# Kernel tuning notes

Measured on AMD Instinct MI355X. Metric: run time of the kernel, lower is better.

## Reference

```python
import jax, jax.numpy as jnp
import numpy as np

N_CLASSES = 91  # classes 0..90; class 0 (background) is excluded from the mean


def setup_inputs() -> dict:
    key = jax.random.key(0)
    k1, k2 = jax.random.split(key)
    B, H, W = 64, 512, 512
    # label maps with integer class ids in [0, 91); `inputs` stored as float32
    # to mirror the original (compared elementwise against integer i)
    inputs = jax.random.randint(k1, (B, H, W), 0, N_CLASSES).astype(jnp.float32)
    targets = jax.random.randint(k2, (B, H, W), 0, N_CLASSES).astype(jnp.int32)
    return {"inputs": inputs, "targets": targets, "smooth": 1}


def reference(inputs, targets, smooth):
    # Single-pass histogram formulation of the original per-class loop:
    #   intersection_i = #{p : inputs[p]==i and targets[p]==i}
    #   total_i        = #{inputs==i} + #{targets==i}
    #   union_i        = total_i - intersection_i
    n = N_CLASSES
    inp = inputs.reshape(-1).astype(jnp.int32)
    tgt = targets.reshape(-1).astype(jnp.int32)
    cnt_in = jnp.bincount(inp, length=n).astype(jnp.float32)
    cnt_tg = jnp.bincount(tgt, length=n).astype(jnp.float32)
    # positions where prediction == target contribute to that class's intersection;
    # mismatches are routed to a dummy bin n and dropped
    inter = jnp.bincount(jnp.where(inp == tgt, inp, n), length=n + 1)[:n].astype(jnp.float32)
    union = cnt_in + cnt_tg - inter
    smooth_f = jnp.float32(smooth)
    iou = (inter[1:] + smooth_f) / (union[1:] + smooth_f)  # classes 1..n-1
    return jnp.sum(iou) / (n - 1)
```

## Files before the change

### kernel.cpp

```cpp
#include <hip/hip_runtime.h>

#define NCLS 91
#define NHIST (3 * NCLS)
#define NBLK 2048
#define BS 256
#define NWAVE (BS / 64)

__global__ void miou_zero_ws(unsigned int* __restrict__ ws) {
    int i = threadIdx.x;
    if (i < NHIST) ws[i] = 0u;
}

__global__ __launch_bounds__(BS) void miou_hist(const float* __restrict__ inp,
                                                const int* __restrict__ tgt,
                                                unsigned int* __restrict__ ws,
                                                int n4) {
    __shared__ unsigned int h[NWAVE][NHIST];
    for (int i = threadIdx.x; i < NWAVE * NHIST; i += BS)
        ((unsigned int*)h)[i] = 0u;
    __syncthreads();

    const int wave = threadIdx.x >> 6;
    unsigned int* hw = h[wave];

    int tid = blockIdx.x * BS + threadIdx.x;
    int stride = gridDim.x * BS;
    const float4* in4 = (const float4*)inp;
    const int4* tg4 = (const int4*)tgt;

    for (int i = tid; i < n4; i += stride) {
        float4 fv = in4[i];
        int4 tv = tg4[i];
        int a0 = (int)fv.x, a1 = (int)fv.y, a2 = (int)fv.z, a3 = (int)fv.w;
        atomicAdd(&hw[a0], 1u);
        atomicAdd(&hw[a1], 1u);
        atomicAdd(&hw[a2], 1u);
        atomicAdd(&hw[a3], 1u);
        atomicAdd(&hw[NCLS + tv.x], 1u);
        atomicAdd(&hw[NCLS + tv.y], 1u);
        atomicAdd(&hw[NCLS + tv.z], 1u);
        atomicAdd(&hw[NCLS + tv.w], 1u);
        if (a0 == tv.x) atomicAdd(&hw[2 * NCLS + a0], 1u);
        if (a1 == tv.y) atomicAdd(&hw[2 * NCLS + a1], 1u);
        if (a2 == tv.z) atomicAdd(&hw[2 * NCLS + a2], 1u);
        if (a3 == tv.w) atomicAdd(&hw[2 * NCLS + a3], 1u);
    }
    __syncthreads();

    for (int i = threadIdx.x; i < NHIST; i += BS) {
        unsigned int v = 0u;
        #pragma unroll
        for (int w = 0; w < NWAVE; ++w) v += h[w][i];
        if (v) atomicAdd(&ws[i], v);
    }
}

__global__ void miou_finalize(const unsigned int* __restrict__ ws,
                              const int* __restrict__ smooth_p,
                              float* __restrict__ out) {
    int lane = threadIdx.x;
    float s = (float)(*smooth_p);
    float acc = 0.f;
    for (int c = 1 + lane; c < NCLS; c += 64) {
        float ci = (float)ws[c];
        float ct = (float)ws[NCLS + c];
        float it = (float)ws[2 * NCLS + c];
        float un = ci + ct - it;
        acc += (it + s) / (un + s);
    }
    #pragma unroll
    for (int off = 32; off; off >>= 1) acc += __shfl_down(acc, off);
    if (lane == 0) out[0] = acc / (float)(NCLS - 1);
}

extern "C" void kernel_launch(void* const* d_in, const int* in_sizes, int n_in,
                              void* d_out, int out_size, void* d_ws, size_t ws_size,
                              hipStream_t stream) {
    const float* inp = (const float*)d_in[0];
    const int* tgt = (const int*)d_in[1];
    const int* smooth_p = (const int*)d_in[2];
    float* out = (float*)d_out;
    unsigned int* ws = (unsigned int*)d_ws;

    int n = in_sizes[0];
    int n4 = n >> 2;

    miou_zero_ws<<<1, 512, 0, stream>>>(ws);
    miou_hist<<<NBLK, BS, 0, stream>>>(inp, tgt, ws, n4);
    miou_finalize<<<1, 64, 0, stream>>>(ws, smooth_p, out);
}
```

Measured before the change: 172.1 us.

## Replicate shared histograms per lane and pack intersection into high half

Replaces the per-wave shared histograms with 16 lane-replicated copies padded to stride 17, so lanes hitting the same class land on different LDS banks and addresses. This cuts atomic conflicts between lanes. The intersection count is packed into the upper 16 bits of the input-class counter, which removes four conditional atomics per iteration. The zeroing kernel is replaced by hipMemsetAsync. Per-block counts must stay below 65536 per slot for the packing to remain correct, which holds with this grid size.

```diff
diff --git a/kernel.cpp b/kernel.cpp
--- a/kernel.cpp
+++ b/kernel.cpp
@@ -4,24 +4,20 @@
 #define NHIST (3 * NCLS)
 #define NBLK 2048
 #define BS 256
-#define NWAVE (BS / 64)
-
-__global__ void miou_zero_ws(unsigned int* __restrict__ ws) {
-    int i = threadIdx.x;
-    if (i < NHIST) ws[i] = 0u;
-}
+#define R 16
+#define RP 17
 
 __global__ __launch_bounds__(BS) void miou_hist(const float* __restrict__ inp,
                                                 const int* __restrict__ tgt,
                                                 unsigned int* __restrict__ ws,
                                                 int n4) {
-    __shared__ unsigned int h[NWAVE][NHIST];
-    for (int i = threadIdx.x; i < NWAVE * NHIST; i += BS)
-        ((unsigned int*)h)[i] = 0u;
+    __shared__ unsigned int h[2 * NCLS * RP];
+    for (int i = threadIdx.x; i < 2 * NCLS * RP; i += BS) h[i] = 0u;
     __syncthreads();
 
-    const int wave = threadIdx.x >> 6;
-    unsigned int* hw = h[wave];
+    const int c = threadIdx.x & (R - 1);
+    unsigned int* hin = h;
+    unsigned int* htg = h + NCLS * RP;
 
     int tid = blockIdx.x * BS + threadIdx.x;
     int stride = gridDim.x * BS;
@@ -32,26 +28,30 @@
         float4 fv = in4[i];
         int4 tv = tg4[i];
         int a0 = (int)fv.x, a1 = (int)fv.y, a2 = (int)fv.z, a3 = (int)fv.w;
-        atomicAdd(&hw[a0], 1u);
-        atomicAdd(&hw[a1], 1u);
-        atomicAdd(&hw[a2], 1u);
-        atomicAdd(&hw[a3], 1u);
-        atomicAdd(&hw[NCLS + tv.x], 1u);
-        atomicAdd(&hw[NCLS + tv.y], 1u);
-        atomicAdd(&hw[NCLS + tv.z], 1u);
-        atomicAdd(&hw[NCLS + tv.w], 1u);
-        if (a0 == tv.x) atomicAdd(&hw[2 * NCLS + a0], 1u);
-        if (a1 == tv.y) atomicAdd(&hw[2 * NCLS + a1], 1u);
-        if (a2 == tv.z) atomicAdd(&hw[2 * NCLS + a2], 1u);
-        if (a3 == tv.w) atomicAdd(&hw[2 * NCLS + a3], 1u);
+        atomicAdd(&hin[a0 * RP + c], 1u + (a0 == tv.x ? 0x10000u : 0u));
+        atomicAdd(&hin[a1 * RP + c], 1u + (a1 == tv.y ? 0x10000u : 0u));
+        atomicAdd(&hin[a2 * RP + c], 1u + (a2 == tv.z ? 0x10000u : 0u));
+        atomicAdd(&hin[a3 * RP + c], 1u + (a3 == tv.w ? 0x10000u : 0u));
+        atomicAdd(&htg[tv.x * RP + c], 1u);
+        atomicAdd(&htg[tv.y * RP + c], 1u);
+        atomicAdd(&htg[tv.z * RP + c], 1u);
+        atomicAdd(&htg[tv.w * RP + c], 1u);
     }
     __syncthreads();
 
-    for (int i = threadIdx.x; i < NHIST; i += BS) {
+    for (int i = threadIdx.x; i < 2 * NCLS; i += BS) {
         unsigned int v = 0u;
+        const unsigned int* p = h + i * RP;
         #pragma unroll
-        for (int w = 0; w < NWAVE; ++w) v += h[w][i];
-        if (v) atomicAdd(&ws[i], v);
+        for (int k = 0; k < R; ++k) v += p[k];
+        if (i < NCLS) {
+            unsigned int lo = v & 0xFFFFu;
+            unsigned int hiw = v >> 16;
+            if (lo) atomicAdd(&ws[i], lo);
+            if (hiw) atomicAdd(&ws[2 * NCLS + i], hiw);
+        } else {
+            if (v) atomicAdd(&ws[NCLS + (i - NCLS)], v);
+        }
     }
 }
 
@@ -61,10 +61,10 @@
     int lane = threadIdx.x;
     float s = (float)(*smooth_p);
     float acc = 0.f;
-    for (int c = 1 + lane; c < NCLS; c += 64) {
-        float ci = (float)ws[c];
-        float ct = (float)ws[NCLS + c];
-        float it = (float)ws[2 * NCLS + c];
+    for (int cc = 1 + lane; cc < NCLS; cc += 64) {
+        float ci = (float)ws[cc];
+        float ct = (float)ws[NCLS + cc];
+        float it = (float)ws[2 * NCLS + cc];
         float un = ci + ct - it;
         acc += (it + s) / (un + s);
     }
@@ -85,7 +85,7 @@
     int n = in_sizes[0];
     int n4 = n >> 2;
 
-    miou_zero_ws<<<1, 512, 0, stream>>>(ws);
+    hipMemsetAsync(ws, 0, NHIST * sizeof(unsigned int), stream);
     miou_hist<<<NBLK, BS, 0, stream>>>(inp, tgt, ws, n4);
     miou_finalize<<<1, 64, 0, stream>>>(ws, smooth_p, out);
 }
```

Result: slower. 193.6 us (+12.5%).
